# Kernel tuning notes

Measured on AMD Instinct MI355X. Metric: run time of the kernel, lower is better.

## Reference

```python
import jax, jax.numpy as jnp
import numpy as np

VOCAB, EBD, ATT_H, R, T, IMG_C = 50257, 512, 512, 196, 1024, 512


def setup_inputs() -> dict:
    key = jax.random.key(0)
    ks = jax.random.split(key, 10)
    question = jax.random.randint(ks[0], (T,), 0, VOCAB)
    img_feat = jax.random.normal(ks[1], (R, IMG_C), dtype=jnp.float32)
    emb_table = (jax.random.normal(ks[2], (VOCAB, EBD), dtype=jnp.float32) * 0.02).at[0].set(0.0)  # padding_idx=0
    W_img = jax.random.normal(ks[3], (EBD, IMG_C), dtype=jnp.float32) * (1.0 / np.sqrt(IMG_C))
    b_img = jnp.zeros((EBD,), dtype=jnp.float32)
    W_ai = jax.random.normal(ks[4], (ATT_H, EBD), dtype=jnp.float32) * (1.0 / np.sqrt(EBD))  # att_img, no bias
    W_aw = jax.random.normal(ks[5], (ATT_H, EBD), dtype=jnp.float32) * (1.0 / np.sqrt(EBD))  # att_word
    b_aw = jnp.zeros((ATT_H,), dtype=jnp.float32)
    w_att = jax.random.normal(ks[6], (ATT_H,), dtype=jnp.float32) * (1.0 / np.sqrt(ATT_H))  # att -> scalar
    b_att = jnp.zeros((), dtype=jnp.float32)
    return {"question": question, "img_feat": img_feat, "emb_table": emb_table,
            "W_img": W_img, "b_img": b_img, "W_ai": W_ai, "W_aw": W_aw,
            "b_aw": b_aw, "w_att": w_att, "b_att": b_att}


def reference(question, img_feat, emb_table, W_img, b_img, W_ai, W_aw, b_aw, w_att, b_att):
    # img_feature = relu(Linear(512 -> ebd)(vgg_regions));  [R, EBD]
    img = jax.nn.relu(img_feat @ W_img.T + b_img)
    # per-word embeddings  [T, EBD]
    E = emb_table[question]
    # additive attention: tanh(attImg[r] + attWord[t]) . w_att + b_att  -> [T, R]
    AI = img @ W_ai.T                       # [R, H]
    AW = E @ W_aw.T + b_aw                  # [T, H]
    scores = jnp.einsum('trh,h->tr', jnp.tanh(AI[None, :, :] + AW[:, None, :]), w_att) + b_att
    w = jax.nn.softmax(scores, axis=-1)     # softmax over regions, [T, R]
    # weighted sum of img features, divided by n_regions (faithful to original)
    ctx = (w @ img) / img.shape[0]          # [T, EBD]
    # attedInput: concat(new_img_feature, word_emd)  [T, 2*EBD]
    return jnp.concatenate([ctx, E], axis=-1)
```

## Files before the change

### kernel.cpp

```cpp
#include <hip/hip_runtime.h>

#define PRESCALE 2.8853900817779268f

typedef short s16;
typedef unsigned short u16;
typedef unsigned int u32;
typedef __attribute__((ext_vector_type(8))) short short8v;
typedef __attribute__((ext_vector_type(4))) float f4;

#if defined(__has_builtin)
#if __has_builtin(__builtin_amdgcn_exp2f)
#define EXP2(x) __builtin_amdgcn_exp2f(x)
#endif
#endif
#ifndef EXP2
#define EXP2(x) exp2f(x)
#endif
#define RCP(x) __builtin_amdgcn_rcpf(x)

__device__ inline u16 f2bf(float f){
  union{u32 i; float f;} v; v.f = f;
  u32 r = v.i + 0x7fffu + ((v.i >> 16) & 1u);
  return (u16)(r >> 16);
}

__global__ __launch_bounds__(256) void k_prep(
    const float* __restrict__ W_img, const float* __restrict__ W_ai,
    const float* __restrict__ W_aw,  const float* __restrict__ img_feat,
    const int* __restrict__ question, const float* __restrict__ emb,
    s16* __restrict__ Wb, s16* __restrict__ Xb, s16* __restrict__ Eb,
    float* __restrict__ out){
  const int g = blockIdx.x*256 + threadIdx.x;
  if (g < 196608){
    const int i = g*4, w = i >> 18;
    const float sc = (w == 0) ? 1.f : PRESCALE;
    const float* src = (w==0) ? W_img : ((w==1) ? W_ai : W_aw);
    float4 v = *reinterpret_cast<const float4*>(src + (i & 262143));
    ushort4 o; o.x=f2bf(v.x*sc); o.y=f2bf(v.y*sc); o.z=f2bf(v.z*sc); o.w=f2bf(v.w*sc);
    *reinterpret_cast<ushort4*>(Wb + i) = o;
  } else if (g < 229376){
    const int i = (g - 196608)*4;
    ushort4 o = make_ushort4(0,0,0,0);
    if ((i >> 9) < 196){
      float4 v = *reinterpret_cast<const float4*>(img_feat + i);
      o.x=f2bf(v.x); o.y=f2bf(v.y); o.z=f2bf(v.z); o.w=f2bf(v.w);
    }
    *reinterpret_cast<ushort4*>(Xb + i) = o;
  } else {
    const int i = (g - 229376)*4;
    const int t = i >> 9, c = i & 511;
    float4 v = *reinterpret_cast<const float4*>(emb + (size_t)question[t]*512 + c);
    *reinterpret_cast<float4*>(out + (size_t)t*1024 + 512 + c) = v;
    ushort4 o; o.x=f2bf(v.x); o.y=f2bf(v.y); o.z=f2bf(v.z); o.w=f2bf(v.w);
    *reinterpret_cast<ushort4*>(Eb + i) = o;
  }
}

__device__ inline void mfma_core(const s16* __restrict__ A, const s16* __restrict__ B,
                                 int m0, int n0, int lr, int lg, f4 acc[2][2]){
  const s16* pa0 = A + (size_t)(m0 + lr)*512 + lg*8;
  const s16* pa1 = pa0 + 16*512;
  const s16* pb0 = B + (size_t)(n0 + lr)*512 + lg*8;
  const s16* pb1 = pb0 + 16*512;
  #pragma unroll 4
  for (int k = 0; k < 512; k += 32){
    short8v a0 = *reinterpret_cast<const short8v*>(pa0 + k);
    short8v a1 = *reinterpret_cast<const short8v*>(pa1 + k);
    short8v b0 = *reinterpret_cast<const short8v*>(pb0 + k);
    short8v b1 = *reinterpret_cast<const short8v*>(pb1 + k);
    acc[0][0] = __builtin_amdgcn_mfma_f32_16x16x32_bf16(a0, b0, acc[0][0], 0, 0, 0);
    acc[0][1] = __builtin_amdgcn_mfma_f32_16x16x32_bf16(a0, b1, acc[0][1], 0, 0, 0);
    acc[1][0] = __builtin_amdgcn_mfma_f32_16x16x32_bf16(a1, b0, acc[1][0], 0, 0, 0);
    acc[1][1] = __builtin_amdgcn_mfma_f32_16x16x32_bf16(a1, b1, acc[1][1], 0, 0, 0);
  }
}

__global__ __launch_bounds__(256) void k_mfma_imgaw(
    const s16* __restrict__ Xb, const s16* __restrict__ Wb_img,
    const s16* __restrict__ Wb_aw, const s16* __restrict__ Eb,
    const float* __restrict__ b_img, const float* __restrict__ b_aw,
    float* __restrict__ img, s16* __restrict__ img_b,
    float* __restrict__ AWT4){
  const int tid = threadIdx.x, w = tid>>6, l = tid&63;
  const int lr = l & 15, lg = l >> 4;
  f4 acc[2][2] = {};
  if (blockIdx.x < 32){
    const int m0 = (blockIdx.x >> 3)*64 + (w>>1)*32;
    const int n0 = (blockIdx.x & 7)*64 + (w&1)*32;
    mfma_core(Xb, Wb_img, m0, n0, lr, lg, acc);
    #pragma unroll
    for (int i = 0; i < 2; ++i){
      #pragma unroll
      for (int j = 0; j < 2; ++j){
        const int nn = n0 + j*16 + lr;
        const float bc = b_img[nn];
        #pragma unroll
        for (int p = 0; p < 4; ++p){
          const int mm = m0 + i*16 + lg*4 + p;
          float v = fmaxf(acc[i][j][p] + bc, 0.f);
          img[(size_t)mm*512 + nn] = v;
          img_b[(size_t)mm*512 + nn] = (s16)f2bf(v);
        }
      }
    }
  } else {
    const int blk = blockIdx.x - 32;
    const int m0 = (blk >> 4)*64 + (w>>1)*32;
    const int n0 = (blk & 15)*64 + (w&1)*32;
    mfma_core(Wb_aw, Eb, m0, n0, lr, lg, acc);
    #pragma unroll
    for (int i = 0; i < 2; ++i){
      const int mb = m0 + i*16 + lg*4;
      const float br = b_aw[mb] * PRESCALE;
      #pragma unroll
      for (int j = 0; j < 2; ++j){
        const int nn = n0 + j*16 + lr;
        f4 o;
        #pragma unroll
        for (int p = 0; p < 4; ++p)
          o[p] = acc[i][j][p] + b_aw[mb+p]*PRESCALE;
        *reinterpret_cast<f4*>(AWT4 + (size_t)(mb>>2)*4096 + nn*4) = o;
      }
      (void)br;
    }
  }
}

__global__ __launch_bounds__(256) void k_mfma_ai(
    const s16* __restrict__ img_b, const s16* __restrict__ Wb_ai,
    float* __restrict__ AI){
  const int tid = threadIdx.x, w = tid>>6, l = tid&63;
  const int lr = l & 15, lg = l >> 4;
  const int m0 = (blockIdx.x >> 3)*64 + (w>>1)*32;
  const int n0 = (blockIdx.x & 7)*64 + (w&1)*32;
  f4 acc[2][2] = {};
  mfma_core(img_b, Wb_ai, m0, n0, lr, lg, acc);
  #pragma unroll
  for (int i = 0; i < 2; ++i)
    #pragma unroll
    for (int j = 0; j < 2; ++j){
      const int nn = n0 + j*16 + lr;
      #pragma unroll
      for (int p = 0; p < 4; ++p){
        const int mm = m0 + i*16 + lg*4 + p;
        AI[(size_t)mm*512 + nn] = acc[i][j][p];
      }
    }
}

__global__ __launch_bounds__(512) void k_score(
    const float* __restrict__ AI, const float* __restrict__ AWT4,
    const float* __restrict__ w_att, float* __restrict__ ST){
  __shared__ float ais[8][512];
  __shared__ float ws[512];
  const int tid = threadIdx.x, w = tid>>6, lane = tid&63;
  const int r0 = blockIdx.x*8;
  for (int i = tid; i < 8*128; i += 512)
    reinterpret_cast<float4*>(&ais[0][0])[i] =
        reinterpret_cast<const float4*>(AI + (size_t)r0*512)[i];
  if (tid < 128)
    reinterpret_cast<float4*>(ws)[tid] = reinterpret_cast<const float4*>(w_att)[tid];
  __syncthreads();
  const int r = r0 + w;
  const int t = blockIdx.y*64 + lane;
  const float* __restrict__ ap = AWT4 + (size_t)t*4;
  float s0=0.f, s1=0.f, s2=0.f, s3=0.f;
  #pragma unroll 4
  for (int hg = 0; hg < 128; ++hg){
    f4 x  = *reinterpret_cast<const f4*>(ap + (size_t)hg*4096);
    f4 a  = *reinterpret_cast<const f4*>(&ais[w][hg*4]);
    f4 wv = *reinterpret_cast<const f4*>(&ws[hg*4]);
    s0 += wv.x * RCP(EXP2(a.x + x.x) + 1.f);
    s1 += wv.y * RCP(EXP2(a.y + x.y) + 1.f);
    s2 += wv.z * RCP(EXP2(a.z + x.z) + 1.f);
    s3 += wv.w * RCP(EXP2(a.w + x.w) + 1.f);
  }
  if (r < 196) ST[(size_t)r*1024 + t] = (s0+s1)+(s2+s3);
}

__global__ __launch_bounds__(256) void k_ctx(
    const float* __restrict__ ST, const float* __restrict__ img,
    float* __restrict__ out){
  __shared__ float wgt[196][16];
  __shared__ float red[16][16];
  const int tid = threadIdx.x;
  const int t0 = blockIdx.x*16, e0 = blockIdx.y*64;
  const int rs = tid>>4, tl = tid&15;

  float m = 1e30f;
  for (int k = 0; k < 13; ++k){
    const int r = rs + 16*k;
    if (r < 196) m = fminf(m, ST[(size_t)r*1024 + t0 + tl]);
  }
  red[rs][tl] = m;
  __syncthreads();
  if (tid < 16){
    float mm = red[0][tid];
    #pragma unroll
    for (int i = 1; i < 16; ++i) mm = fminf(mm, red[i][tid]);
    red[0][tid] = mm;
  }
  __syncthreads();
  const float mt = red[0][tl];
  float sum = 0.f;
  for (int k = 0; k < 13; ++k){
    const int r = rs + 16*k;
    if (r < 196){
      float p = EXP2(PRESCALE*(mt - ST[(size_t)r*1024 + t0 + tl]));
      wgt[r][tl] = p;
      sum += p;
    }
  }
  __syncthreads();
  red[rs][tl] = sum;
  __syncthreads();
  if (tid < 16){
    float ss = 0.f;
    #pragma unroll
    for (int i = 0; i < 16; ++i) ss += red[i][tid];
    red[0][tid] = 1.f / (ss * 196.f);
  }
  __syncthreads();
  const float inv = red[0][tl];
  for (int k = 0; k < 13; ++k){
    const int r = rs + 16*k;
    if (r < 196) wgt[r][tl] *= inv;
  }
  __syncthreads();

  const int e = e0 + (tid & 63), tq = tid >> 6;
  float acc[4] = {0.f, 0.f, 0.f, 0.f};
  const float* ip = img + e;
  #pragma unroll 4
  for (int r = 0; r < 196; ++r){
    const float f = ip[(size_t)r*512];
    float4 w4 = *reinterpret_cast<const float4*>(&wgt[r][tq*4]);
    acc[0] += w4.x*f; acc[1] += w4.y*f; acc[2] += w4.z*f; acc[3] += w4.w*f;
  }
  #pragma unroll
  for (int j = 0; j < 4; ++j)
    out[(size_t)(t0 + tq*4 + j)*1024 + e] = acc[j];
}

extern "C" void kernel_launch(void* const* d_in, const int* in_sizes, int n_in,
                              void* d_out, int out_size, void* d_ws, size_t ws_size,
                              hipStream_t stream) {
  const int*   question = (const int*)d_in[0];
  const float* img_feat = (const float*)d_in[1];
  const float* emb      = (const float*)d_in[2];
  const float* W_img    = (const float*)d_in[3];
  const float* b_img    = (const float*)d_in[4];
  const float* W_ai     = (const float*)d_in[5];
  const float* W_aw     = (const float*)d_in[6];
  const float* b_aw     = (const float*)d_in[7];
  const float* w_att    = (const float*)d_in[8];
  float* out = (float*)d_out;

  char* ws = (char*)d_ws;
  s16*   Wb    = (s16*)(ws);
  s16*   Xb    = (s16*)(ws + 1572864);
  s16*   Eb    = (s16*)(ws + 1835008);
  float* img   = (float*)(ws + 2883584);
  s16*   img_b = (s16*)(ws + 3407872);
  float* AI    = (float*)(ws + 3670016);
  float* AWT4  = (float*)(ws + 4194304);
  float* ST    = (float*)(ws + 6291456);

  hipLaunchKernelGGL(k_prep, dim3(1408), dim3(256), 0, stream,
                     W_img, W_ai, W_aw, img_feat, question, emb, Wb, Xb, Eb, out);
  hipLaunchKernelGGL(k_mfma_imgaw, dim3(160), dim3(256), 0, stream,
                     Xb, Wb, Wb + 2*262144, Eb, b_img, b_aw, img, img_b, AWT4);
  hipLaunchKernelGGL(k_mfma_ai, dim3(32), dim3(256), 0, stream,
                     img_b, Wb + 262144, AI);
  hipLaunchKernelGGL(k_score, dim3(25,16), dim3(512), 0, stream, AI, AWT4, w_att, ST);
  hipLaunchKernelGGL(k_ctx,   dim3(64,8),  dim3(256), 0, stream, ST, img, out);
}
```

Before: 82.70 us.

## Fuse pipeline into cooperative persistent kernel and fold AI GEMM into score phase

Merges the five launches into one cooperative kernel whose phases are separated by grid syncs, removing per-launch overhead and gaps between kernels. The separate AI GEMM kernel is dropped: each score block recomputes its 16-row AI tile with MFMA straight into shared memory, and each wave now handles two regions. A fallback path issues four ordinary launches if the cooperative launch fails. The cost is redundant AI computation across blocks, grid-wide barrier overhead, and score blocks cut from 512 to 256 threads.

Result: slower. 263.8 us (+219.0%).

```diff
diff --git a/kernel.cpp b/kernel.cpp
--- a/kernel.cpp
+++ b/kernel.cpp
@@ -1,4 +1,7 @@
 #include <hip/hip_runtime.h>
+#include <hip/hip_cooperative_groups.h>
+
+namespace cg = cooperative_groups;
 
 #define PRESCALE 2.8853900817779268f
 
@@ -24,35 +27,42 @@
   return (u16)(r >> 16);
 }
 
-__global__ __launch_bounds__(256) void k_prep(
-    const float* __restrict__ W_img, const float* __restrict__ W_ai,
-    const float* __restrict__ W_aw,  const float* __restrict__ img_feat,
-    const int* __restrict__ question, const float* __restrict__ emb,
-    s16* __restrict__ Wb, s16* __restrict__ Xb, s16* __restrict__ Eb,
-    float* __restrict__ out){
-  const int g = blockIdx.x*256 + threadIdx.x;
-  if (g < 196608){
-    const int i = g*4, w = i >> 18;
-    const float sc = (w == 0) ? 1.f : PRESCALE;
-    const float* src = (w==0) ? W_img : ((w==1) ? W_ai : W_aw);
-    float4 v = *reinterpret_cast<const float4*>(src + (i & 262143));
-    ushort4 o; o.x=f2bf(v.x*sc); o.y=f2bf(v.y*sc); o.z=f2bf(v.z*sc); o.w=f2bf(v.w*sc);
-    *reinterpret_cast<ushort4*>(Wb + i) = o;
-  } else if (g < 229376){
-    const int i = (g - 196608)*4;
-    ushort4 o = make_ushort4(0,0,0,0);
-    if ((i >> 9) < 196){
-      float4 v = *reinterpret_cast<const float4*>(img_feat + i);
-      o.x=f2bf(v.x); o.y=f2bf(v.y); o.z=f2bf(v.z); o.w=f2bf(v.w);
-    }
-    *reinterpret_cast<ushort4*>(Xb + i) = o;
-  } else {
-    const int i = (g - 229376)*4;
-    const int t = i >> 9, c = i & 511;
-    float4 v = *reinterpret_cast<const float4*>(emb + (size_t)question[t]*512 + c);
-    *reinterpret_cast<float4*>(out + (size_t)t*1024 + 512 + c) = v;
-    ushort4 o; o.x=f2bf(v.x); o.y=f2bf(v.y); o.z=f2bf(v.z); o.w=f2bf(v.w);
-    *reinterpret_cast<ushort4*>(Eb + i) = o;
+struct Ptrs {
+  const int* question; const float* img_feat; const float* emb;
+  const float* W_img; const float* b_img; const float* W_ai;
+  const float* W_aw; const float* b_aw; const float* w_att;
+  float* out;
+  s16* Wb; s16* Xb; s16* Eb; float* img; s16* img_b;
+  float* AWT4; float* ST;
+};
+
+#define SMEM_BYTES 34816
+
+__device__ void phase_prep(const Ptrs& P, int bx, int tid, int nblk){
+  for (int g = bx*256 + tid; g < 360448; g += nblk*256){
+    if (g < 196608){
+      const int i = g*4, w = i >> 18;
+      const float sc = (w == 0) ? 1.f : PRESCALE;
+      const float* src = (w==0) ? P.W_img : ((w==1) ? P.W_ai : P.W_aw);
+      float4 v = *reinterpret_cast<const float4*>(src + (i & 262143));
+      ushort4 o; o.x=f2bf(v.x*sc); o.y=f2bf(v.y*sc); o.z=f2bf(v.z*sc); o.w=f2bf(v.w*sc);
+      *reinterpret_cast<ushort4*>(P.Wb + i) = o;
+    } else if (g < 229376){
+      const int i = (g - 196608)*4;
+      ushort4 o = make_ushort4(0,0,0,0);
+      if ((i >> 9) < 196){
+        float4 v = *reinterpret_cast<const float4*>(P.img_feat + i);
+        o.x=f2bf(v.x); o.y=f2bf(v.y); o.z=f2bf(v.z); o.w=f2bf(v.w);
+      }
+      *reinterpret_cast<ushort4*>(P.Xb + i) = o;
+    } else {
+      const int i = (g - 229376)*4;
+      const int t = i >> 9, c = i & 511;
+      float4 v = *reinterpret_cast<const float4*>(P.emb + (size_t)P.question[t]*512 + c);
+      *reinterpret_cast<float4*>(P.out + (size_t)t*1024 + 512 + c) = v;
+      ushort4 o; o.x=f2bf(v.x); o.y=f2bf(v.y); o.z=f2bf(v.z); o.w=f2bf(v.w);
+      *reinterpret_cast<ushort4*>(P.Eb + i) = o;
+    }
   }
 }
 
@@ -75,122 +85,112 @@
   }
 }
 
-__global__ __launch_bounds__(256) void k_mfma_imgaw(
-    const s16* __restrict__ Xb, const s16* __restrict__ Wb_img,
-    const s16* __restrict__ Wb_aw, const s16* __restrict__ Eb,
-    const float* __restrict__ b_img, const float* __restrict__ b_aw,
-    float* __restrict__ img, s16* __restrict__ img_b,
-    float* __restrict__ AWT4){
-  const int tid = threadIdx.x, w = tid>>6, l = tid&63;
-  const int lr = l & 15, lg = l >> 4;
+__device__ void phase_gemms(const Ptrs& P, int bx, int tid){
+  if (bx >= 160) return;
+  const int w = tid>>6, l = tid&63, lr = l&15, lg = l>>4;
   f4 acc[2][2] = {};
-  if (blockIdx.x < 32){
-    const int m0 = (blockIdx.x >> 3)*64 + (w>>1)*32;
-    const int n0 = (blockIdx.x & 7)*64 + (w&1)*32;
-    mfma_core(Xb, Wb_img, m0, n0, lr, lg, acc);
+  if (bx < 32){
+    const int m0 = (bx >> 3)*64 + (w>>1)*32;
+    const int n0 = (bx & 7)*64 + (w&1)*32;
+    mfma_core(P.Xb, P.Wb, m0, n0, lr, lg, acc);
     #pragma unroll
     for (int i = 0; i < 2; ++i){
       #pragma unroll
       for (int j = 0; j < 2; ++j){
         const int nn = n0 + j*16 + lr;
-        const float bc = b_img[nn];
+        const float bc = P.b_img[nn];
         #pragma unroll
         for (int p = 0; p < 4; ++p){
           const int mm = m0 + i*16 + lg*4 + p;
           float v = fmaxf(acc[i][j][p] + bc, 0.f);
-          img[(size_t)mm*512 + nn] = v;
-          img_b[(size_t)mm*512 + nn] = (s16)f2bf(v);
+          P.img[(size_t)mm*512 + nn] = v;
+          P.img_b[(size_t)mm*512 + nn] = (s16)f2bf(v);
         }
       }
     }
   } else {
-    const int blk = blockIdx.x - 32;
+    const int blk = bx - 32;
     const int m0 = (blk >> 4)*64 + (w>>1)*32;
     const int n0 = (blk & 15)*64 + (w&1)*32;
-    mfma_core(Wb_aw, Eb, m0, n0, lr, lg, acc);
+    mfma_core(P.Wb + 524288, P.Eb, m0, n0, lr, lg, acc);
     #pragma unroll
     for (int i = 0; i < 2; ++i){
       const int mb = m0 + i*16 + lg*4;
-      const float br = b_aw[mb] * PRESCALE;
       #pragma unroll
       for (int j = 0; j < 2; ++j){
         const int nn = n0 + j*16 + lr;
         f4 o;
         #pragma unroll
         for (int p = 0; p < 4; ++p)
-          o[p] = acc[i][j][p] + b_aw[mb+p]*PRESCALE;
-        *reinterpret_cast<f4*>(AWT4 + (size_t)(mb>>2)*4096 + nn*4) = o;
+          o[p] = acc[i][j][p] + P.b_aw[mb+p]*PRESCALE;
+        *reinterpret_cast<f4*>(P.AWT4 + (size_t)(mb>>2)*4096 + nn*4) = o;
       }
-      (void)br;
-    }
-  }
-}
-
-__global__ __launch_bounds__(256) void k_mfma_ai(
-    const s16* __restrict__ img_b, const s16* __restrict__ Wb_ai,
-    float* __restrict__ AI){
-  const int tid = threadIdx.x, w = tid>>6, l = tid&63;
-  const int lr = l & 15, lg = l >> 4;
-  const int m0 = (blockIdx.x >> 3)*64 + (w>>1)*32;
-  const int n0 = (blockIdx.x & 7)*64 + (w&1)*32;
-  f4 acc[2][2] = {};
-  mfma_core(img_b, Wb_ai, m0, n0, lr, lg, acc);
-  #pragma unroll
-  for (int i = 0; i < 2; ++i)
-    #pragma unroll
-    for (int j = 0; j < 2; ++j){
-      const int nn = n0 + j*16 + lr;
+    }
+  }
+}
+
+__device__ void phase_score(const Ptrs& P, char* smemc, int bx, int tid){
+  if (bx >= 400) return;
+  float* ais = (float*)smemc;
+  float* wsh = (float*)smemc + 8192;
+  const int w = tid>>6, l = tid&63, lr = l&15, lg = l>>4;
+  const int rq = bx>>4, tq = bx&15;
+  const int arow0 = (rq>>1)*16;
+  {
+    const s16* pa = P.img_b + (size_t)(arow0+lr)*512 + lg*8;
+    const s16* pb = P.Wb + 262144 + (size_t)(w*128+lr)*512 + lg*8;
+    f4 acc[8] = {};
+    #pragma unroll 2
+    for (int ks = 0; ks < 16; ++ks){
+      short8v a = *reinterpret_cast<const short8v*>(pa + ks*32);
       #pragma unroll
-      for (int p = 0; p < 4; ++p){
-        const int mm = m0 + i*16 + lg*4 + p;
-        AI[(size_t)mm*512 + nn] = acc[i][j][p];
+      for (int nf = 0; nf < 8; ++nf){
+        short8v b = *reinterpret_cast<const short8v*>(pb + ks*32 + nf*8192);
+        acc[nf] = __builtin_amdgcn_mfma_f32_16x16x32_bf16(a, b, acc[nf], 0, 0, 0);
       }
     }
-}
-
-__global__ __launch_bounds__(512) void k_score(
-    const float* __restrict__ AI, const float* __restrict__ AWT4,
-    const float* __restrict__ w_att, float* __restrict__ ST){
-  __shared__ float ais[8][512];
-  __shared__ float ws[512];
-  const int tid = threadIdx.x, w = tid>>6, lane = tid&63;
-  const int r0 = blockIdx.x*8;
-  for (int i = tid; i < 8*128; i += 512)
-    reinterpret_cast<float4*>(&ais[0][0])[i] =
-        reinterpret_cast<const float4*>(AI + (size_t)r0*512)[i];
+    #pragma unroll
+    for (int nf = 0; nf < 8; ++nf)
+      #pragma unroll
+      for (int p = 0; p < 4; ++p)
+        ais[(size_t)(lg*4+p)*512 + w*128 + nf*16 + lr] = acc[nf][p];
+  }
   if (tid < 128)
-    reinterpret_cast<float4*>(ws)[tid] = reinterpret_cast<const float4*>(w_att)[tid];
-  __syncthreads();
-  const int r = r0 + w;
-  const int t = blockIdx.y*64 + lane;
-  const float* __restrict__ ap = AWT4 + (size_t)t*4;
+    reinterpret_cast<float4*>(wsh)[tid] = reinterpret_cast<const float4*>(P.w_att)[tid];
+  __syncthreads();
+
+  const int roff = (rq&1)*8;
+  const float* a0 = ais + (size_t)(roff + w*2)*512;
+  const float* a1 = a0 + 512;
+  const int t = tq*64 + l;
+  const float* ap = P.AWT4 + (size_t)t*4;
   float s0=0.f, s1=0.f, s2=0.f, s3=0.f;
   #pragma unroll 4
   for (int hg = 0; hg < 128; ++hg){
     f4 x  = *reinterpret_cast<const f4*>(ap + (size_t)hg*4096);
-    f4 a  = *reinterpret_cast<const f4*>(&ais[w][hg*4]);
-    f4 wv = *reinterpret_cast<const f4*>(&ws[hg*4]);
-    s0 += wv.x * RCP(EXP2(a.x + x.x) + 1.f);
-    s1 += wv.y * RCP(EXP2(a.y + x.y) + 1.f);
-    s2 += wv.z * RCP(EXP2(a.z + x.z) + 1.f);
-    s3 += wv.w * RCP(EXP2(a.w + x.w) + 1.f);
-  }
-  if (r < 196) ST[(size_t)r*1024 + t] = (s0+s1)+(s2+s3);
-}
-
-__global__ __launch_bounds__(256) void k_ctx(
-    const float* __restrict__ ST, const float* __restrict__ img,
-    float* __restrict__ out){
-  __shared__ float wgt[196][16];
-  __shared__ float red[16][16];
-  const int tid = threadIdx.x;
-  const int t0 = blockIdx.x*16, e0 = blockIdx.y*64;
+    f4 av = *reinterpret_cast<const f4*>(a0 + hg*4);
+    f4 bv = *reinterpret_cast<const f4*>(a1 + hg*4);
+    f4 wv = *reinterpret_cast<const f4*>(wsh + hg*4);
+    s0 += wv.x*RCP(EXP2(av.x+x.x)+1.f) + wv.y*RCP(EXP2(av.y+x.y)+1.f);
+    s1 += wv.z*RCP(EXP2(av.z+x.z)+1.f) + wv.w*RCP(EXP2(av.w+x.w)+1.f);
+    s2 += wv.x*RCP(EXP2(bv.x+x.x)+1.f) + wv.y*RCP(EXP2(bv.y+x.y)+1.f);
+    s3 += wv.z*RCP(EXP2(bv.z+x.z)+1.f) + wv.w*RCP(EXP2(bv.w+x.w)+1.f);
+  }
+  const int r = rq*8 + w*2;
+  if (r < 196)     P.ST[(size_t)r*1024 + t]     = s0+s1;
+  if (r+1 < 196)   P.ST[(size_t)(r+1)*1024 + t] = s2+s3;
+}
+
+__device__ void phase_ctx(const Ptrs& P, char* smemc, int bx, int tid){
+  float (*wgt)[16] = (float(*)[16])smemc;
+  float (*red)[16] = (float(*)[16])(smemc + 12544);
+  const int t0 = (bx>>3)*16, e0 = (bx&7)*64;
   const int rs = tid>>4, tl = tid&15;
 
   float m = 1e30f;
   for (int k = 0; k < 13; ++k){
     const int r = rs + 16*k;
-    if (r < 196) m = fminf(m, ST[(size_t)r*1024 + t0 + tl]);
+    if (r < 196) m = fminf(m, P.ST[(size_t)r*1024 + t0 + tl]);
   }
   red[rs][tl] = m;
   __syncthreads();
@@ -206,7 +206,7 @@
   for (int k = 0; k < 13; ++k){
     const int r = rs + 16*k;
     if (r < 196){
-      float p = EXP2(PRESCALE*(mt - ST[(size_t)r*1024 + t0 + tl]));
+      float p = EXP2(PRESCALE*(mt - P.ST[(size_t)r*1024 + t0 + tl]));
       wgt[r][tl] = p;
       sum += p;
     }
@@ -230,7 +230,7 @@
 
   const int e = e0 + (tid & 63), tq = tid >> 6;
   float acc[4] = {0.f, 0.f, 0.f, 0.f};
-  const float* ip = img + e;
+  const float* ip = P.img + e;
   #pragma unroll 4
   for (int r = 0; r < 196; ++r){
     const float f = ip[(size_t)r*512];
@@ -239,39 +239,67 @@
   }
   #pragma unroll
   for (int j = 0; j < 4; ++j)
-    out[(size_t)(t0 + tq*4 + j)*1024 + e] = acc[j];
+    P.out[(size_t)(t0 + tq*4 + j)*1024 + e] = acc[j];
+}
+
+__global__ __launch_bounds__(256, 2) void k_mega(Ptrs P){
+  __shared__ __align__(16) char smem[SMEM_BYTES];
+  cg::grid_group g = cg::this_grid();
+  const int bx = blockIdx.x, tid = threadIdx.x;
+  phase_prep(P, bx, tid, gridDim.x);
+  g.sync();
+  phase_gemms(P, bx, tid);
+  g.sync();
+  phase_score(P, smem, bx, tid);
+  g.sync();
+  phase_ctx(P, smem, bx, tid);
+}
+
+__global__ __launch_bounds__(256) void k_p0(Ptrs P){
+  phase_prep(P, blockIdx.x, threadIdx.x, gridDim.x);
+}
+__global__ __launch_bounds__(256) void k_p1(Ptrs P){
+  phase_gemms(P, blockIdx.x, threadIdx.x);
+}
+__global__ __launch_bounds__(256) void k_p2(Ptrs P){
+  __shared__ __align__(16) char smem[SMEM_BYTES];
+  phase_score(P, smem, blockIdx.x, threadIdx.x);
+}
+__global__ __launch_bounds__(256) void k_p3(Ptrs P){
+  __shared__ __align__(16) char smem[SMEM_BYTES];
+  phase_ctx(P, smem, blockIdx.x, threadIdx.x);
 }
 
 extern "C" void kernel_launch(void* const* d_in, const int* in_sizes, int n_in,
                               void* d_out, int out_size, void* d_ws, size_t ws_size,
                               hipStream_t stream) {
-  const int*   question = (const int*)d_in[0];
-  const float* img_feat = (const float*)d_in[1];
-  const float* emb      = (const float*)d_in[2];
-  const float* W_img    = (const float*)d_in[3];
-  const float* b_img    = (const float*)d_in[4];
-  const float* W_ai     = (const float*)d_in[5];
-  const float* W_aw     = (const float*)d_in[6];
-  const float* b_aw     = (const float*)d_in[7];
-  const float* w_att    = (const float*)d_in[8];
-  float* out = (float*)d_out;
-
   char* ws = (char*)d_ws;
-  s16*   Wb    = (s16*)(ws);
-  s16*   Xb    = (s16*)(ws + 1572864);
-  s16*   Eb    = (s16*)(ws + 1835008);
-  float* img   = (float*)(ws + 2883584);
-  s16*   img_b = (s16*)(ws + 3407872);
-  float* AI    = (float*)(ws + 3670016);
-  float* AWT4  = (float*)(ws + 4194304);
-  float* ST    = (float*)(ws + 6291456);
-
-  hipLaunchKernelGGL(k_prep, dim3(1408), dim3(256), 0, stream,
-                     W_img, W_ai, W_aw, img_feat, question, emb, Wb, Xb, Eb, out);
-  hipLaunchKernelGGL(k_mfma_imgaw, dim3(160), dim3(256), 0, stream,
-                     Xb, Wb, Wb + 2*262144, Eb, b_img, b_aw, img, img_b, AWT4);
-  hipLaunchKernelGGL(k_mfma_ai, dim3(32), dim3(256), 0, stream,
-                     img_b, Wb + 262144, AI);
-  hipLaunchKernelGGL(k_score, dim3(25,16), dim3(512), 0, stream, AI, AWT4, w_att, ST);
-  hipLaunchKernelGGL(k_ctx,   dim3(64,8),  dim3(256), 0, stream, ST, img, out);
-}
+  Ptrs P;
+  P.question = (const int*)d_in[0];
+  P.img_feat = (const float*)d_in[1];
+  P.emb      = (const float*)d_in[2];
+  P.W_img    = (const float*)d_in[3];
+  P.b_img    = (const float*)d_in[4];
+  P.W_ai     = (const float*)d_in[5];
+  P.W_aw     = (const float*)d_in[6];
+  P.b_aw     = (const float*)d_in[7];
+  P.w_att    = (const float*)d_in[8];
+  P.out   = (float*)d_out;
+  P.Wb    = (s16*)(ws);
+  P.Xb    = (s16*)(ws + 1572864);
+  P.Eb    = (s16*)(ws + 1835008);
+  P.img   = (float*)(ws + 2883584);
+  P.img_b = (s16*)(ws + 3407872);
+  P.AWT4  = (float*)(ws + 3670016);
+  P.ST    = (float*)(ws + 5767168);
+
+  void* args[] = { (void*)&P };
+  hipError_t e = hipLaunchCooperativeKernel((const void*)k_mega, dim3(512), dim3(256),
+                                            args, 0, stream);
+  if (e != hipSuccess){
+    hipLaunchKernelGGL(k_p0, dim3(512), dim3(256), 0, stream, P);
+    hipLaunchKernelGGL(k_p1, dim3(160), dim3(256), 0, stream, P);
+    hipLaunchKernelGGL(k_p2, dim3(400), dim3(256), 0, stream, P);
+    hipLaunchKernelGGL(k_p3, dim3(512), dim3(256), 0, stream, P);
+  }
+}
```
